# Kernel optimization log

Hardware: AMD Instinct MI355X
Metric: run time of the kernel (lower is better)

The kernel has to match this reference:

```python
import jax, jax.numpy as jnp
import numpy as np

B, S = 4, 1024          # 4 prefill sequences of length 1024 (cu_seqlens equal-length)
D_MODEL = 2048
N_HEADS = 32
N_KV_HEADS = 8
HEAD_DIM = D_MODEL // N_HEADS          # 64
GROUPS = N_HEADS // N_KV_HEADS         # 4
ROPE_THETA = 10000.0
SCALE = HEAD_DIM ** -0.5


def setup_inputs() -> dict:
    key = jax.random.key(0)
    ks = jax.random.split(key, 6)
    T = B * S
    hidden_states = jax.random.normal(ks[0], (T, D_MODEL), jnp.float32)
    # rotary tables: positions restart per sequence (prefill)
    pos = jnp.tile(jnp.arange(S, dtype=jnp.float32), B)            # [T]
    inv_freq = 1.0 / (ROPE_THETA ** (jnp.arange(0, HEAD_DIM, 2, dtype=jnp.float32) / HEAD_DIM))
    freqs = pos[:, None] * inv_freq[None, :]                        # [T, HEAD_DIM/2]
    cos, sin = jnp.cos(freqs), jnp.sin(freqs)
    std = D_MODEL ** -0.5
    Wq = jax.random.normal(ks[1], (D_MODEL, N_HEADS * HEAD_DIM), jnp.float32) * std
    Wk = jax.random.normal(ks[2], (D_MODEL, N_KV_HEADS * HEAD_DIM), jnp.float32) * std
    Wv = jax.random.normal(ks[3], (D_MODEL, N_KV_HEADS * HEAD_DIM), jnp.float32) * std
    Wo = jax.random.normal(ks[4], (N_HEADS * HEAD_DIM, D_MODEL), jnp.float32) * std
    return {"hidden_states": hidden_states, "cos": cos, "sin": sin,
            "Wq": Wq, "Wk": Wk, "Wv": Wv, "Wo": Wo}


def _rope(x, cos, sin):
    # NeoX-style rotary: x [T, H, D], cos/sin [T, D/2]
    half = x.shape[-1] // 2
    x1, x2 = x[..., :half], x[..., half:]
    c, s = cos[:, None, :], sin[:, None, :]
    return jnp.concatenate([x1 * c - x2 * s, x2 * c + x1 * s], axis=-1)


def reference(hidden_states, cos, sin, Wq, Wk, Wv, Wo):
    T = hidden_states.shape[0]
    q = (hidden_states @ Wq).reshape(T, N_HEADS, HEAD_DIM)
    k = (hidden_states @ Wk).reshape(T, N_KV_HEADS, HEAD_DIM)
    v = (hidden_states @ Wv).reshape(T, N_KV_HEADS, HEAD_DIM)
    q = _rope(q, cos, sin)
    k = _rope(k, cos, sin)
    # equal-length varlen prefill -> [B, S, H, D]
    q = q.reshape(B, S, N_HEADS, HEAD_DIM)
    k = jnp.repeat(k.reshape(B, S, N_KV_HEADS, HEAD_DIM), GROUPS, axis=2)  # GQA expand
    v = jnp.repeat(v.reshape(B, S, N_KV_HEADS, HEAD_DIM), GROUPS, axis=2)
    scores = jnp.einsum("bqhd,bkhd->bhqk", q, k) * SCALE
    causal = jnp.tril(jnp.ones((S, S), dtype=bool))
    scores = jnp.where(causal[None, None], scores, jnp.finfo(scores.dtype).min)
    probs = jax.nn.softmax(scores, axis=-1)
    attn = jnp.einsum("bhqk,bkhd->bqhd", probs, v).reshape(T, N_HEADS * HEAD_DIM)
    return attn @ Wo
```

## Files before the change

### kernel.cpp

```cpp
#include <hip/hip_runtime.h>
#include <type_traits>


typedef __bf16 bf16x8 __attribute__((ext_vector_type(8)));
typedef __bf16 bf16x4 __attribute__((ext_vector_type(4)));
typedef float f32x4 __attribute__((ext_vector_type(4)));
typedef unsigned short u16;
typedef unsigned int u32;

#define DEVI __device__ __forceinline__

DEVI u16 f2bf(float f) {
  u32 u = __builtin_bit_cast(u32, f);
  u += 0x7FFF + ((u >> 16) & 1);
  return (u16)(u >> 16);
}

DEVI void ld16_lds(const void* g, void* l) {
  __builtin_amdgcn_global_load_lds((const __attribute__((address_space(1))) u32*)g,
                                   (__attribute__((address_space(3))) u32*)l, 16, 0, 0);
}

template <int N> DEVI void waitvm() {
  if constexpr (N == 0) asm volatile("s_waitcnt vmcnt(0)" ::: "memory");
  else if constexpr (N == 6) asm volatile("s_waitcnt vmcnt(6)" ::: "memory");
  else if constexpr (N == 8) asm volatile("s_waitcnt vmcnt(8)" ::: "memory");
  else static_assert(N == 0, "unsupported vmcnt");
}
DEVI void lgkm0() {
  asm volatile("s_waitcnt lgkmcnt(0)" ::: "memory");
  __builtin_amdgcn_sched_barrier(0);
}
DEVI void barrier() { __builtin_amdgcn_s_barrier(); }

__global__ __launch_bounds__(256) void convert_f32_bf16(const float* __restrict__ src,
                                                        u16* __restrict__ dst, int n4) {
  int i = blockIdx.x * 256 + threadIdx.x;
  if (i >= n4) return;
  float4 v = ((const float4*)src)[i];
  ushort4 o;
  o.x = f2bf(v.x); o.y = f2bf(v.y); o.z = f2bf(v.z); o.w = f2bf(v.w);
  ((ushort4*)dst)[i] = o;
}

__global__ __launch_bounds__(256) void trans_f32_bf16(const float* __restrict__ src,
                                                      u16* __restrict__ dst, int R, int C,
                                                      float scale) {
  __shared__ float tile[32][33];
  int c0 = blockIdx.x * 32, r0 = blockIdx.y * 32;
  int tx = threadIdx.x & 31, ty = threadIdx.x >> 5;
#pragma unroll
  for (int i = 0; i < 32; i += 8)
    tile[ty + i][tx] = src[(size_t)(r0 + ty + i) * C + (c0 + tx)];
  __syncthreads();
#pragma unroll
  for (int i = 0; i < 32; i += 8)
    dst[(size_t)(c0 + ty + i) * R + (r0 + tx)] = f2bf(tile[tx][ty + i] * scale);
}

template <typename OutT, bool ROPE, int BN>
__global__ __launch_bounds__(512, 2) void gemm8(const u16* __restrict__ A,
                                                const u16* __restrict__ BT,
                                                OutT* __restrict__ C, int M, int N, int K,
                                                const float* __restrict__ cs,
                                                const float* __restrict__ sn) {
  constexpr int WN = BN / 64;
  constexpr int NH = WN / 2;
  constexpr int LB = BN / 128;
  constexpr int VMW = 4 + 2 * LB;
  __shared__ u16 As[2][256 * 64];
  __shared__ u16 Bs[2][BN * 64];
  const int tid = threadIdx.x;
  const int lane = tid & 63, wave = tid >> 6;
  const int quad = lane >> 4, l16 = lane & 15;

  const int nwg = gridDim.x * gridDim.y;
  const int bid = blockIdx.y * gridDim.x + blockIdx.x;
  const int swz = (bid & 7) * (nwg >> 3) + (bid >> 3);
  const int m0 = (swz / gridDim.x) * 256, n0 = (swz % gridDim.x) * BN;
  const int wr = wave >> 2, wc = wave & 3;

  f32x4 acc[8][WN] = {};

  auto stageA = [&](int t, int h) {
    u16* D = &As[t & 1][h * 8192];
    const u16* G = A + (size_t)m0 * K + t * 64;
#pragma unroll
    for (int i = 0; i < 2; ++i) {
      int id = i * 512 + tid;
      int row = h * 128 + (id >> 3), ch = id & 7;
      ld16_lds(G + (size_t)row * K + (ch ^ (row & 7)) * 8, D + id * 8);
    }
  };
  auto stageB = [&](int t, int h) {
    u16* D = &Bs[t & 1][h * (BN / 2) * 64];
    const u16* G = BT + (size_t)n0 * K + t * 64;
#pragma unroll
    for (int i = 0; i < LB; ++i) {
      int id = i * 512 + tid;
      int row = h * (BN / 2) + (id >> 3), ch = id & 7;
      ld16_lds(G + (size_t)row * K + (ch ^ (row & 7)) * 8, D + id * 8);
    }
  };

  bf16x8 af[4][2], bv0[NH][2], bv1[NH][2];
  auto ldA = [&](int msub, int d) {
#pragma unroll
    for (int i = 0; i < 4; ++i)
#pragma unroll
      for (int ks = 0; ks < 2; ++ks) {
        int r = wr * 128 + msub * 64 + i * 16 + l16;
        af[i][ks] = *(const bf16x8*)&As[d][r * 64 + (((ks * 4 + quad) ^ (r & 7)) * 8)];
      }
  };
  auto ldB = [&](bf16x8 (&bv)[NH][2], int nsub, int d) {
#pragma unroll
    for (int j = 0; j < NH; ++j)
#pragma unroll
      for (int ks = 0; ks < 2; ++ks) {
        int rb = wc * (16 * WN) + (nsub * NH + j) * 16 + l16;
        bv[j][ks] = *(const bf16x8*)&Bs[d][rb * 64 + (((ks * 4 + quad) ^ (rb & 7)) * 8)];
      }
  };
  auto mm = [&](const bf16x8 (&bv)[NH][2], int mo, int no) {
    __builtin_amdgcn_s_setprio(1);
#pragma unroll
    for (int i = 0; i < 4; ++i)
#pragma unroll
      for (int j = 0; j < NH; ++j)
#pragma unroll
        for (int ks = 0; ks < 2; ++ks)
          acc[mo + i][no + j] =
              __builtin_amdgcn_mfma_f32_16x16x32_bf16(af[i][ks], bv[j][ks], acc[mo + i][no + j], 0, 0, 0);
    __builtin_amdgcn_s_setprio(0);
  };

  const int NT = K / 64;

  stageA(0, 0); stageA(0, 1); stageB(0, 0); stageB(0, 1);
  stageA(1, 0); stageA(1, 1); stageB(1, 0); stageB(1, 1);
  waitvm<VMW>();
  barrier();

#pragma unroll 1
  for (int T = 0; T < NT; T += 2) {
    const bool pf = (T + 2 < NT);
    ldA(0, 0); ldB(bv0, 0, 0);
    barrier(); lgkm0();
    mm(bv0, 0, 0);
    barrier();

    ldB(bv1, 1, 0);
    barrier(); lgkm0();
    mm(bv1, 0, NH);
    barrier();

    ldA(1, 0);
    if (pf) { stageB(T + 2, 0); stageB(T + 2, 1); }
    barrier(); lgkm0();
    mm(bv1, 4, NH);
    barrier();

    if (pf) {
      stageA(T + 2, 0); stageA(T + 2, 1);
      waitvm<VMW>();
    } else {
      waitvm<0>();
    }
    barrier();
    __builtin_amdgcn_sched_barrier(0);
    mm(bv0, 4, 0);
    barrier();

    ldA(0, 1); ldB(bv0, 0, 1);
    barrier(); lgkm0();
    mm(bv0, 0, 0);
    barrier();

    ldB(bv1, 1, 1);
    barrier(); lgkm0();
    mm(bv1, 0, NH);
    barrier();

    ldA(1, 1);
    if (pf) { stageB(T + 3, 0); stageB(T + 3, 1); }
    barrier(); lgkm0();
    mm(bv1, 4, NH);
    barrier();

    if (pf) {
      stageA(T + 3, 0); stageA(T + 3, 1);
      waitvm<VMW>();
      barrier();
      __builtin_amdgcn_sched_barrier(0);
      mm(bv0, 4, 0);
      barrier();
    } else {
      mm(bv0, 4, 0);
    }
  }

  if constexpr (ROPE) {
    if (n0 + wc * (16 * WN) < 2560) {
#pragma unroll
      for (int i = 0; i < 8; i++) {
        int t0 = m0 + wr * 128 + i * 16 + quad * 4;
#pragma unroll
        for (int jj = 0; jj < 2; jj++) {
          int d = jj * 16 + l16;
#pragma unroll
          for (int r = 0; r < 4; r++) {
            float cv = cs[(size_t)(t0 + r) * 32 + d];
            float sv = sn[(size_t)(t0 + r) * 32 + d];
            float x1 = acc[i][jj][r], x2 = acc[i][jj + 2][r];
            acc[i][jj][r] = x1 * cv - x2 * sv;
            acc[i][jj + 2][r] = x2 * cv + x1 * sv;
          }
        }
      }
    }
  }

#pragma unroll
  for (int i = 0; i < 8; i++) {
    int row = m0 + wr * 128 + i * 16 + quad * 4;
#pragma unroll
    for (int j = 0; j < WN; j++) {
      int col = n0 + wc * (16 * WN) + j * 16 + l16;
#pragma unroll
      for (int r = 0; r < 4; r++) {
        size_t off = (size_t)(row + r) * N + col;
        if constexpr (sizeof(OutT) == 2) C[off] = f2bf(acc[i][j][r]);
        else C[off] = acc[i][j][r];
      }
    }
  }
}

__global__ __launch_bounds__(256) void vkt_build(const u16* __restrict__ qkv,
                                                 u16* __restrict__ vkt) {
  __shared__ u16 Vn[128 * 64];
  const int kt = blockIdx.x, kvh = blockIdx.y, b = blockIdx.z;
  const int tid = threadIdx.x;
  const u16* src = qkv + ((size_t)b * 1024 + kt * 128) * 3072 + 2560 + kvh * 64;
  {
    int tok = tid >> 1, hf = tid & 1;
    const uint4* s4 = (const uint4*)(src + (size_t)tok * 3072 + hf * 32);
    uint4* d4 = (uint4*)&Vn[tok * 64 + hf * 32];
#pragma unroll
    for (int j = 0; j < 4; j++) d4[j] = s4[j];
  }
  __syncthreads();
  u16* img = vkt + ((((size_t)b * 8 + kvh) * 8 + kt) << 13);
#pragma unroll
  for (int i = 0; i < 4; i++) {
    int c = tid * 4 + i;
    int dd = c >> 4, chsw = c & 15;
    int ch = chsw ^ (dd & 15);
    u16 tmp[8];
#pragma unroll
    for (int p = 0; p < 8; p++) {
      int col = ch * 8 + p;
      int g = col >> 5, kl = col & 31;
      int kph = ((kl >> 2) & 1) * 16 + ((kl >> 4) & 1) * 8 + ((kl >> 3) & 1) * 4 + (kl & 3);
      tmp[p] = Vn[(g * 32 + kph) * 64 + dd];
    }
    *(uint4*)&img[c * 8] = *(const uint4*)tmp;
  }
}

__global__ __launch_bounds__(256, 2) void flash_attn(const u16* __restrict__ qkv,
                                                     const u16* __restrict__ vkt,
                                                     u16* __restrict__ attn) {
  __shared__ u16 Ks[2][128 * 64];
  __shared__ u16 VT[2][64 * 128];

  const int tid = threadIdx.x;
  const int lane = tid & 63, wave = tid >> 6;
  const int quad = lane >> 4, l16 = lane & 15;
  const int qtA = blockIdx.x, qtB = 7 - blockIdx.x;
  const int h = blockIdx.y, b = blockIdx.z, kvh = h >> 2;
  const size_t tokBase = (size_t)b * 1024;
  const int qcol = h * 64, kcol = 2048 + kvh * 64;
  const int srow = tid >> 3, spc = tid & 7, ssc = spc ^ (srow & 7);

  auto stageK = [&](const u16* gbase, u16* L) {
#pragma unroll
    for (int i = 0; i < 4; i++)
      ld16_lds(gbase + (size_t)(srow + i * 32) * 3072 + ssc * 8, &L[tid * 8 + i * 2048]);
  };
  const u16* vimg = vkt + (((size_t)b * 8 + kvh) << 16);
  auto stageV = [&](int kt, u16* L) {
    const u16* g = vimg + ((size_t)kt << 13);
#pragma unroll
    for (int i = 0; i < 4; i++)
      ld16_lds(g + i * 2048 + tid * 8, &L[tid * 8 + i * 2048]);
  };

  stageK(qkv + (tokBase + qtA * 128) * 3072 + qcol, Ks[0]);
  stageK(qkv + (tokBase + qtB * 128) * 3072 + qcol, Ks[1]);
  __syncthreads();
  bf16x8 qfA[2][2], qfB[2][2];
#pragma unroll
  for (int nq = 0; nq < 2; nq++) {
    int qrow = wave * 32 + nq * 16 + l16;
#pragma unroll
    for (int ks = 0; ks < 2; ks++) {
      int c = (ks * 4 + quad) ^ (qrow & 7);
      qfA[nq][ks] = *(const bf16x8*)&Ks[0][qrow * 64 + c * 8];
      qfB[nq][ks] = *(const bf16x8*)&Ks[1][qrow * 64 + c * 8];
    }
  }
  __syncthreads();

  float lA[2] = {0.f, 0.f}, lB[2] = {0.f, 0.f};
  f32x4 oA[4][2] = {}, oB[4][2] = {};

  auto proc = [&](const bf16x8 (&kf)[2][2], const bf16x8 (&va)[4], const bf16x8 (&qf)[2][2],
                  f32x4 (&o)[4][2], float (&lacc)[2], bool msk, int c) {
    f32x4 s[2][2] = {};
#pragma unroll
    for (int mkl = 0; mkl < 2; mkl++)
#pragma unroll
      for (int ks = 0; ks < 2; ks++) {
        s[0][mkl] = __builtin_amdgcn_mfma_f32_16x16x32_bf16(kf[mkl][ks], qf[0][ks], s[0][mkl], 0, 0, 0);
        s[1][mkl] = __builtin_amdgcn_mfma_f32_16x16x32_bf16(kf[mkl][ks], qf[1][ks], s[1][mkl], 0, 0, 0);
      }
    if (msk) {
#pragma unroll
      for (int nq = 0; nq < 2; nq++) {
        int q = wave * 32 + nq * 16 + l16;
#pragma unroll
        for (int mkl = 0; mkl < 2; mkl++)
#pragma unroll
          for (int r = 0; r < 4; r++)
            if ((c * 2 + mkl) * 16 + quad * 4 + r > q) s[nq][mkl][r] = -3e38f;
      }
    }
    bf16x8 pf[2];
#pragma unroll
    for (int nq = 0; nq < 2; nq++) {
      float a0 = 0.f;
#pragma unroll
      for (int mkl = 0; mkl < 2; mkl++)
#pragma unroll
        for (int r = 0; r < 4; r++) {
          float p = __builtin_amdgcn_exp2f(s[nq][mkl][r]);
          s[nq][mkl][r] = p;
          a0 += p;
        }
      lacc[nq] += a0;
      pf[nq][0] = (__bf16)s[nq][0][0]; pf[nq][1] = (__bf16)s[nq][0][1];
      pf[nq][2] = (__bf16)s[nq][0][2]; pf[nq][3] = (__bf16)s[nq][0][3];
      pf[nq][4] = (__bf16)s[nq][1][0]; pf[nq][5] = (__bf16)s[nq][1][1];
      pf[nq][6] = (__bf16)s[nq][1][2]; pf[nq][7] = (__bf16)s[nq][1][3];
    }
#pragma unroll
    for (int md = 0; md < 4; md++) {
      o[md][0] = __builtin_amdgcn_mfma_f32_16x16x32_bf16(va[md], pf[0], o[md][0], 0, 0, 0);
      o[md][1] = __builtin_amdgcn_mfma_f32_16x16x32_bf16(va[md], pf[1], o[md][1], 0, 0, 0);
    }
  };

  stageK(qkv + tokBase * 3072 + kcol, Ks[0]);
  stageV(0, VT[0]);

  for (int kt = 0; kt <= qtB; kt++) {
    const int cur = kt & 1;
    __syncthreads();
    if (kt < qtB) {
      stageK(qkv + (tokBase + (kt + 1) * 128) * 3072 + kcol, Ks[1 - cur]);
      stageV(kt + 1, VT[1 - cur]);
    }
    const bool doA = (kt <= qtA), mA = (kt == qtA), mB = (kt == qtB);
    const u16* K = Ks[cur];
    const u16* V = VT[cur];
#pragma unroll
    for (int c = 0; c < 4; c++) {
      bf16x8 kf[2][2];
#pragma unroll
      for (int mkl = 0; mkl < 2; mkl++) {
        int krow = (c * 2 + mkl) * 16 + l16;
#pragma unroll
        for (int ks = 0; ks < 2; ks++)
          kf[mkl][ks] = *(const bf16x8*)&K[krow * 64 + ((ks * 4 + quad) ^ (krow & 7)) * 8];
      }
      bf16x8 va[4];
#pragma unroll
      for (int md = 0; md < 4; md++) {
        int dd = md * 16 + l16;
        va[md] = *(const bf16x8*)&V[dd * 128 + ((c * 4 + quad) ^ l16) * 8];
      }
      proc(kf, va, qfB, oB, lB, mB, c);
      if (doA) proc(kf, va, qfA, oA, lA, mA, c);
    }
  }

  auto epilogue = [&](const f32x4 (&o)[4][2], const float (&lacc)[2], int qt_tile) {
#pragma unroll
    for (int nq = 0; nq < 2; nq++) {
      float l = lacc[nq];
      l += __shfl_xor(l, 16);
      l += __shfl_xor(l, 32);
      float inv = 1.0f / l;
      int t = qt_tile * 128 + wave * 32 + nq * 16 + l16;
      size_t rowOff = (tokBase + t) * 2048 + qcol;
#pragma unroll
      for (int md = 0; md < 4; md++) {
        bf16x4 w;
        w[0] = (__bf16)(o[md][nq][0] * inv);
        w[1] = (__bf16)(o[md][nq][1] * inv);
        w[2] = (__bf16)(o[md][nq][2] * inv);
        w[3] = (__bf16)(o[md][nq][3] * inv);
        *(bf16x4*)&attn[rowOff + md * 16 + quad * 4] = w;
      }
    }
  };
  epilogue(oB, lB, qtB);
  epilogue(oA, lA, qtA);
}

extern "C" void kernel_launch(void* const* d_in, const int* in_sizes, int n_in,
                              void* d_out, int out_size, void* d_ws, size_t ws_size,
                              hipStream_t stream) {
  const float* hs = (const float*)d_in[0];
  const float* cs = (const float*)d_in[1];
  const float* sn = (const float*)d_in[2];
  const float* Wq = (const float*)d_in[3];
  const float* Wk = (const float*)d_in[4];
  const float* Wv = (const float*)d_in[5];
  const float* Wo = (const float*)d_in[6];
  float* out = (float*)d_out;

  char* ws = (char*)d_ws;
  u16* hsB   = (u16*)(ws);
  u16* vkt   = (u16*)(ws);
  u16* wqkvT = (u16*)(ws + 16777216);
  u16* woT   = (u16*)(ws + 29360128);
  u16* qkv   = (u16*)(ws + 37748736);
  u16* attnB = (u16*)(ws + 62914560);

  const float QSCALE = 0.18033688011112042f;

  convert_f32_bf16<<<8192, 256, 0, stream>>>(hs, hsB, 4096 * 2048 / 4);
  trans_f32_bf16<<<dim3(64, 64), 256, 0, stream>>>(Wq, wqkvT, 2048, 2048, QSCALE);
  trans_f32_bf16<<<dim3(16, 64), 256, 0, stream>>>(Wk, wqkvT + (size_t)2048 * 2048, 2048, 512, 1.0f);
  trans_f32_bf16<<<dim3(16, 64), 256, 0, stream>>>(Wv, wqkvT + (size_t)2560 * 2048, 2048, 512, 1.0f);
  trans_f32_bf16<<<dim3(64, 64), 256, 0, stream>>>(Wo, woT, 2048, 2048, 1.0f);

  gemm8<u16, true, 256><<<dim3(12, 16), 512, 0, stream>>>(
      hsB, wqkvT, qkv, 4096, 3072, 2048, cs, sn);
  vkt_build<<<dim3(8, 8, 4), 256, 0, stream>>>(qkv, vkt);
  flash_attn<<<dim3(4, 32, 4), 256, 0, stream>>>(qkv, vkt, attnB);
  gemm8<float, false, 128><<<dim3(16, 16), 512, 0, stream>>>(
      attnB, woT, out, 4096, 2048, 2048, nullptr, nullptr);
}
```

Baseline: 268.3 us.

## Retile QKV GEMM to 192-wide N tiles and move RoPE into V-transpose kernel

The QKV projection GEMM now uses BN=192, giving a 16x16 grid of 256 workgroups instead of 192, so more CUs get work on a 256-CU device. Because a 192-wide tile no longer lines up with head boundaries, the fused RoPE epilogue is removed. RoPE is now applied in place on the bf16 Q/K output by the V-transpose kernel, which is renamed rope_vkt. That adds an extra read-modify-write pass over Q and K in bf16, rounding before the rotation rather than after. Flash attention also raises wave priority around its MFMA blocks.

```diff
diff --git a/kernel.cpp b/kernel.cpp
--- a/kernel.cpp
+++ b/kernel.cpp
@@ -24,7 +24,7 @@
 template <int N> DEVI void waitvm() {
   if constexpr (N == 0) asm volatile("s_waitcnt vmcnt(0)" ::: "memory");
   else if constexpr (N == 6) asm volatile("s_waitcnt vmcnt(6)" ::: "memory");
-  else if constexpr (N == 8) asm volatile("s_waitcnt vmcnt(8)" ::: "memory");
+  else if constexpr (N == 7) asm volatile("s_waitcnt vmcnt(7)" ::: "memory");
   else static_assert(N == 0, "unsupported vmcnt");
 }
 DEVI void lgkm0() {
@@ -58,16 +58,14 @@
     dst[(size_t)(c0 + ty + i) * R + (r0 + tx)] = f2bf(tile[tx][ty + i] * scale);
 }
 
-template <typename OutT, bool ROPE, int BN>
+template <typename OutT, int BN>
 __global__ __launch_bounds__(512, 2) void gemm8(const u16* __restrict__ A,
                                                 const u16* __restrict__ BT,
-                                                OutT* __restrict__ C, int M, int N, int K,
-                                                const float* __restrict__ cs,
-                                                const float* __restrict__ sn) {
+                                                OutT* __restrict__ C, int M, int N, int K) {
   constexpr int WN = BN / 64;
-  constexpr int NH = WN / 2;
-  constexpr int LB = BN / 128;
-  constexpr int VMW = 4 + 2 * LB;
+  constexpr int NH0 = (WN + 1) / 2;
+  constexpr int NH1 = WN - NH0;
+  constexpr int VMW = 4 + WN;
   __shared__ u16 As[2][256 * 64];
   __shared__ u16 Bs[2][BN * 64];
   const int tid = threadIdx.x;
@@ -92,18 +90,18 @@
       ld16_lds(G + (size_t)row * K + (ch ^ (row & 7)) * 8, D + id * 8);
     }
   };
-  auto stageB = [&](int t, int h) {
-    u16* D = &Bs[t & 1][h * (BN / 2) * 64];
+  auto stageB = [&](int t, int u) {
+    u16* D = &Bs[t & 1][u * 4096];
     const u16* G = BT + (size_t)n0 * K + t * 64;
-#pragma unroll
-    for (int i = 0; i < LB; ++i) {
-      int id = i * 512 + tid;
-      int row = h * (BN / 2) + (id >> 3), ch = id & 7;
-      ld16_lds(G + (size_t)row * K + (ch ^ (row & 7)) * 8, D + id * 8);
-    }
-  };
-
-  bf16x8 af[4][2], bv0[NH][2], bv1[NH][2];
+    int row = u * 64 + (tid >> 3), ch = tid & 7;
+    ld16_lds(G + (size_t)row * K + (ch ^ (row & 7)) * 8, D + tid * 8);
+  };
+  auto stageBall = [&](int t) {
+#pragma unroll
+    for (int u = 0; u < WN; ++u) stageB(t, u);
+  };
+
+  bf16x8 af[4][2], bv0[NH0][2], bv1[NH1][2];
   auto ldA = [&](int msub, int d) {
 #pragma unroll
     for (int i = 0; i < 4; ++i)
@@ -113,52 +111,73 @@
         af[i][ks] = *(const bf16x8*)&As[d][r * 64 + (((ks * 4 + quad) ^ (r & 7)) * 8)];
       }
   };
-  auto ldB = [&](bf16x8 (&bv)[NH][2], int nsub, int d) {
-#pragma unroll
-    for (int j = 0; j < NH; ++j)
+  auto ldB0 = [&](int d) {
+#pragma unroll
+    for (int j = 0; j < NH0; ++j)
 #pragma unroll
       for (int ks = 0; ks < 2; ++ks) {
-        int rb = wc * (16 * WN) + (nsub * NH + j) * 16 + l16;
-        bv[j][ks] = *(const bf16x8*)&Bs[d][rb * 64 + (((ks * 4 + quad) ^ (rb & 7)) * 8)];
-      }
-  };
-  auto mm = [&](const bf16x8 (&bv)[NH][2], int mo, int no) {
+        int rb = wc * (16 * WN) + j * 16 + l16;
+        bv0[j][ks] = *(const bf16x8*)&Bs[d][rb * 64 + (((ks * 4 + quad) ^ (rb & 7)) * 8)];
+      }
+  };
+  auto ldB1 = [&](int d) {
+#pragma unroll
+    for (int j = 0; j < NH1; ++j)
+#pragma unroll
+      for (int ks = 0; ks < 2; ++ks) {
+        int rb = wc * (16 * WN) + (NH0 + j) * 16 + l16;
+        bv1[j][ks] = *(const bf16x8*)&Bs[d][rb * 64 + (((ks * 4 + quad) ^ (rb & 7)) * 8)];
+      }
+  };
+  auto mm0 = [&](int mo) {
     __builtin_amdgcn_s_setprio(1);
 #pragma unroll
     for (int i = 0; i < 4; ++i)
 #pragma unroll
-      for (int j = 0; j < NH; ++j)
+      for (int j = 0; j < NH0; ++j)
 #pragma unroll
         for (int ks = 0; ks < 2; ++ks)
-          acc[mo + i][no + j] =
-              __builtin_amdgcn_mfma_f32_16x16x32_bf16(af[i][ks], bv[j][ks], acc[mo + i][no + j], 0, 0, 0);
+          acc[mo + i][j] =
+              __builtin_amdgcn_mfma_f32_16x16x32_bf16(af[i][ks], bv0[j][ks], acc[mo + i][j], 0, 0, 0);
     __builtin_amdgcn_s_setprio(0);
   };
+  auto mm1 = [&](int mo) {
+    __builtin_amdgcn_s_setprio(1);
+#pragma unroll
+    for (int i = 0; i < 4; ++i)
+#pragma unroll
+      for (int j = 0; j < NH1; ++j)
+#pragma unroll
+        for (int ks = 0; ks < 2; ++ks)
+          acc[mo + i][NH0 + j] =
+              __builtin_amdgcn_mfma_f32_16x16x32_bf16(af[i][ks], bv1[j][ks], acc[mo + i][NH0 + j], 0, 0, 0);
+    __builtin_amdgcn_s_setprio(0);
+  };
 
   const int NT = K / 64;
 
-  stageA(0, 0); stageA(0, 1); stageB(0, 0); stageB(0, 1);
-  stageA(1, 0); stageA(1, 1); stageB(1, 0); stageB(1, 1);
+  stageA(0, 0); stageA(0, 1); stageBall(0);
+  stageA(1, 0); stageA(1, 1); stageBall(1);
   waitvm<VMW>();
   barrier();
 
 #pragma unroll 1
   for (int T = 0; T < NT; T += 2) {
     const bool pf = (T + 2 < NT);
-    ldA(0, 0); ldB(bv0, 0, 0);
+    ldA(0, 0); ldB0(0);
     barrier(); lgkm0();
-    mm(bv0, 0, 0);
-    barrier();
-
-    ldB(bv1, 1, 0);
+    mm0(0);
+    barrier();
+
+    ldB1(0);
     barrier(); lgkm0();
-    mm(bv1, 0, NH);
+    mm1(0);
     barrier();
 
     ldA(1, 0);
-    if (pf) { stageB(T + 2, 0); stageB(T + 2, 1); }
+    if (pf) stageBall(T + 2);
     barrier(); lgkm0();
-    mm(bv1, 4, NH);
+    mm1(4);
     barrier();
 
     if (pf) {
@@ -169,23 +188,23 @@
     }
     barrier();
     __builtin_amdgcn_sched_barrier(0);
-    mm(bv0, 4, 0);
-    barrier();
-
-    ldA(0, 1); ldB(bv0, 0, 1);
+    mm0(4);
+    barrier();
+
+    ldA(0, 1); ldB0(1);
     barrier(); lgkm0();
-    mm(bv0, 0, 0);
-    barrier();
-
-    ldB(bv1, 1, 1);
+    mm0(0);
+    barrier();
+
+    ldB1(1);
     barrier(); lgkm0();
-    mm(bv1, 0, NH);
+    mm1(0);
     barrier();
 
     ldA(1, 1);
-    if (pf) { stageB(T + 3, 0); stageB(T + 3, 1); }
+    if (pf) stageBall(T + 3);
     barrier(); lgkm0();
-    mm(bv1, 4, NH);
+    mm1(4);
     barrier();
 
     if (pf) {
@@ -193,31 +212,10 @@
       waitvm<VMW>();
       barrier();
       __builtin_amdgcn_sched_barrier(0);
-      mm(bv0, 4, 0);
+      mm0(4);
       barrier();
     } else {
-      mm(bv0, 4, 0);
-    }
-  }
-
-  if constexpr (ROPE) {
-    if (n0 + wc * (16 * WN) < 2560) {
-#pragma unroll
-      for (int i = 0; i < 8; i++) {
-        int t0 = m0 + wr * 128 + i * 16 + quad * 4;
-#pragma unroll
-        for (int jj = 0; jj < 2; jj++) {
-          int d = jj * 16 + l16;
-#pragma unroll
-          for (int r = 0; r < 4; r++) {
-            float cv = cs[(size_t)(t0 + r) * 32 + d];
-            float sv = sn[(size_t)(t0 + r) * 32 + d];
-            float x1 = acc[i][jj][r], x2 = acc[i][jj + 2][r];
-            acc[i][jj][r] = x1 * cv - x2 * sv;
-            acc[i][jj + 2][r] = x2 * cv + x1 * sv;
-          }
-        }
-      }
+      mm0(4);
     }
   }
 
@@ -237,12 +235,57 @@
   }
 }
 
-__global__ __launch_bounds__(256) void vkt_build(const u16* __restrict__ qkv,
-                                                 u16* __restrict__ vkt) {
+__global__ __launch_bounds__(256) void rope_vkt(u16* __restrict__ qkv,
+                                                u16* __restrict__ vkt,
+                                                const float* __restrict__ cs,
+                                                const float* __restrict__ sn) {
+  const int kt = blockIdx.x, h = blockIdx.y, b = blockIdx.z;
+  const int tid = threadIdx.x;
+  const size_t tok0 = (size_t)b * 1024 + (size_t)kt * 128;
+
+  {
+    const int r = tid >> 1, hf = tid & 1;
+    const size_t t = tok0 + r;
+    const float* cr = cs + t * 32;
+    const float* sr = sn + t * 32;
+    u16* qrow = qkv + t * 3072 + h * 64;
+    u16* krow = qkv + t * 3072 + 2048 + h * 64;
+#pragma unroll
+    for (int gg = 0; gg < 2; ++gg) {
+      const int g = hf * 2 + gg;
+      float cv[8], sv[8];
+#pragma unroll
+      for (int e = 0; e < 8; ++e) { cv[e] = cr[g * 8 + e]; sv[e] = sr[g * 8 + e]; }
+      {
+        bf16x8 a = *(bf16x8*)&qrow[g * 8];
+        bf16x8 b2 = *(bf16x8*)&qrow[g * 8 + 32];
+#pragma unroll
+        for (int e = 0; e < 8; ++e) {
+          float x1 = (float)a[e], x2 = (float)b2[e];
+          a[e] = (__bf16)(x1 * cv[e] - x2 * sv[e]);
+          b2[e] = (__bf16)(x2 * cv[e] + x1 * sv[e]);
+        }
+        *(bf16x8*)&qrow[g * 8] = a;
+        *(bf16x8*)&qrow[g * 8 + 32] = b2;
+      }
+      if (h < 8) {
+        bf16x8 a = *(bf16x8*)&krow[g * 8];
+        bf16x8 b2 = *(bf16x8*)&krow[g * 8 + 32];
+#pragma unroll
+        for (int e = 0; e < 8; ++e) {
+          float x1 = (float)a[e], x2 = (float)b2[e];
+          a[e] = (__bf16)(x1 * cv[e] - x2 * sv[e]);
+          b2[e] = (__bf16)(x2 * cv[e] + x1 * sv[e]);
+        }
+        *(bf16x8*)&krow[g * 8] = a;
+        *(bf16x8*)&krow[g * 8 + 32] = b2;
+      }
+    }
+  }
+  if (h >= 8) return;
+
   __shared__ u16 Vn[128 * 64];
-  const int kt = blockIdx.x, kvh = blockIdx.y, b = blockIdx.z;
-  const int tid = threadIdx.x;
-  const u16* src = qkv + ((size_t)b * 1024 + kt * 128) * 3072 + 2560 + kvh * 64;
+  const u16* src = qkv + tok0 * 3072 + 2560 + h * 64;
   {
     int tok = tid >> 1, hf = tid & 1;
     const uint4* s4 = (const uint4*)(src + (size_t)tok * 3072 + hf * 32);
@@ -251,7 +294,7 @@
     for (int j = 0; j < 4; j++) d4[j] = s4[j];
   }
   __syncthreads();
-  u16* img = vkt + ((((size_t)b * 8 + kvh) * 8 + kt) << 13);
+  u16* img = vkt + ((((size_t)b * 8 + h) * 8 + kt) << 13);
 #pragma unroll
   for (int i = 0; i < 4; i++) {
     int c = tid * 4 + i;
@@ -319,6 +362,7 @@
   auto proc = [&](const bf16x8 (&kf)[2][2], const bf16x8 (&va)[4], const bf16x8 (&qf)[2][2],
                   f32x4 (&o)[4][2], float (&lacc)[2], bool msk, int c) {
     f32x4 s[2][2] = {};
+    __builtin_amdgcn_s_setprio(1);
 #pragma unroll
     for (int mkl = 0; mkl < 2; mkl++)
 #pragma unroll
@@ -326,6 +370,7 @@
         s[0][mkl] = __builtin_amdgcn_mfma_f32_16x16x32_bf16(kf[mkl][ks], qf[0][ks], s[0][mkl], 0, 0, 0);
         s[1][mkl] = __builtin_amdgcn_mfma_f32_16x16x32_bf16(kf[mkl][ks], qf[1][ks], s[1][mkl], 0, 0, 0);
       }
+    __builtin_amdgcn_s_setprio(0);
     if (msk) {
 #pragma unroll
       for (int nq = 0; nq < 2; nq++) {
@@ -355,11 +400,13 @@
       pf[nq][4] = (__bf16)s[nq][1][0]; pf[nq][5] = (__bf16)s[nq][1][1];
       pf[nq][6] = (__bf16)s[nq][1][2]; pf[nq][7] = (__bf16)s[nq][1][3];
     }
+    __builtin_amdgcn_s_setprio(1);
 #pragma unroll
     for (int md = 0; md < 4; md++) {
       o[md][0] = __builtin_amdgcn_mfma_f32_16x16x32_bf16(va[md], pf[0], o[md][0], 0, 0, 0);
       o[md][1] = __builtin_amdgcn_mfma_f32_16x16x32_bf16(va[md], pf[1], o[md][1], 0, 0, 0);
     }
+    __builtin_amdgcn_s_setprio(0);
   };
 
   stageK(qkv + tokBase * 3072 + kcol, Ks[0]);
@@ -448,10 +495,8 @@
   trans_f32_bf16<<<dim3(16, 64), 256, 0, stream>>>(Wv, wqkvT + (size_t)2560 * 2048, 2048, 512, 1.0f);
   trans_f32_bf16<<<dim3(64, 64), 256, 0, stream>>>(Wo, woT, 2048, 2048, 1.0f);
 
-  gemm8<u16, true, 256><<<dim3(12, 16), 512, 0, stream>>>(
-      hsB, wqkvT, qkv, 4096, 3072, 2048, cs, sn);
-  vkt_build<<<dim3(8, 8, 4), 256, 0, stream>>>(qkv, vkt);
+  gemm8<u16, 192><<<dim3(16, 16), 512, 0, stream>>>(hsB, wqkvT, qkv, 4096, 3072, 2048);
+  rope_vkt<<<dim3(8, 32, 4), 256, 0, stream>>>(qkv, vkt, cs, sn);
   flash_attn<<<dim3(4, 32, 4), 256, 0, stream>>>(qkv, vkt, attnB);
-  gemm8<float, false, 128><<<dim3(16, 16), 512, 0, stream>>>(
-      attnB, woT, out, 4096, 2048, 2048, nullptr, nullptr);
-}
+  gemm8<float, 128><<<dim3(16, 16), 512, 0, stream>>>(attnB, woT, out, 4096, 2048, 2048);
+}
```

Measured after the change: 272.7 us. About the same (+1.6%).
